# Kernel optimization log

Measured on AMD Instinct MI355X. Metric: run time of the kernel, lower is better.

Reference implementation:

```python
import jax, jax.numpy as jnp
import numpy as np

B, S, D, E, R = 8, 4096, 768, 8, 8

def setup_inputs() -> dict:
    key = jax.random.key(0)
    ks = jax.random.split(key, 9)
    sc = 0.02
    return {
        "x":  jax.random.normal(ks[0], (B, S, D), dtype=jnp.float32),
        "Wd": jax.random.normal(ks[1], (E, D, R), dtype=jnp.float32) * sc,
        "bd": jax.random.normal(ks[2], (E, R), dtype=jnp.float32) * sc,
        "Wm": jax.random.normal(ks[3], (E, R, R), dtype=jnp.float32) * sc,
        "bm": jax.random.normal(ks[4], (E, R), dtype=jnp.float32) * sc,
        "Wu": jax.random.normal(ks[5], (E, R, D), dtype=jnp.float32) * sc,
        "bu": jax.random.normal(ks[6], (E, D), dtype=jnp.float32) * sc,
        "Wg": jax.random.normal(ks[7], (D, E), dtype=jnp.float32) * sc,
        "bg": jax.random.normal(ks[8], (E,), dtype=jnp.float32) * sc,
    }

def reference(x, Wd, bd, Wm, bm, Wu, bu, Wg, bg):
    # Gating: softmax over experts. [B,S,E]
    gate = jax.nn.softmax(jnp.einsum('bsd,de->bse', x, Wg) + bg, axis=-1)
    # All experts batched as 3D GEMMs (dropout = identity, eval mode).
    h = jnp.einsum('bsd,edr->bser', x, Wd) + bd            # [B,S,E,R] down
    h = jnp.einsum('bser,erq->bseq', h, Wm) + bm           # [B,S,E,R] mid
    up = jnp.einsum('bser,erd->bsed', h, Wu) + bu          # [B,S,E,D] up
    # Weighted sum over experts.
    return jnp.einsum('bse,bsed->bsd', gate, up)
```

## Files before the change

kernel.cpp:

```cpp
#include <hip/hip_runtime.h>
#include <stdint.h>


typedef short bf16x8 __attribute__((ext_vector_type(8)));
typedef float f32x4 __attribute__((ext_vector_type(4)));

static __device__ __forceinline__ unsigned short f2bf(float f) {
  union { float f; uint32_t u; } v; v.f = f;
  return (unsigned short)((v.u + 0x7fffu + ((v.u >> 16) & 1u)) >> 16);
}

__global__ void prep_weights(const float* __restrict__ Wd, const float* __restrict__ Wg,
                             const float* __restrict__ Wu, const float* __restrict__ bu,
                             unsigned short* __restrict__ w1f, unsigned short* __restrict__ w2f) {
  int tid = blockIdx.x * 256 + threadIdx.x;
  const int N1 = 24 * 5 * 64 * 8;
  if (tid < N1) {
    int i    = tid & 7;
    int lane = (tid >> 3) & 63;
    int fk   = tid >> 9;
    int f = fk % 5, K0 = fk / 5;
    int k = K0 * 32 + (lane >> 4) * 8 + i;
    int j = f * 16 + (lane & 15);
    float val = 0.f;
    if (j < 64)      val = Wd[(size_t)(j >> 3) * 6144 + (size_t)k * 8 + (j & 7)];
    else if (j < 72) val = Wg[(size_t)k * 8 + (j - 64)];
    w1f[tid] = f2bf(val);
  } else {
    int t2 = tid - N1;
    if (t2 >= 48 * 3 * 64 * 8) return;
    int i    = t2 & 7;
    int lane = (t2 >> 3) & 63;
    int tk   = t2 >> 9;
    int K0 = tk % 3, T = tk / 3;
    int k = K0 * 32 + (lane >> 4) * 8 + i;
    int n = T * 16 + (lane & 15);
    float val = 0.f;
    if (k < 64)      val = Wu[(size_t)(k >> 3) * 6144 + (size_t)(k & 7) * 768 + n];
    else if (k < 72) val = bu[(size_t)(k - 64) * 768 + n];
    w2f[t2] = f2bf(val);
  }
}

__global__ __launch_bounds__(256, 8) void moba_fused(
    const float* __restrict__ x,
    const float* __restrict__ bd, const float* __restrict__ Wm,
    const float* __restrict__ bm, const float* __restrict__ bg,
    const unsigned short* __restrict__ w1f, const unsigned short* __restrict__ w2f,
    float* __restrict__ out) {
  __shared__ float Hs[4][16][81];
  __shared__ unsigned int g2s[16][52];

  const int tidx = threadIdx.x;
  const int lane = tidx & 63;
  const int wave = tidx >> 6;
  const int arow = lane & 15;
  const int kgrp = lane >> 4;
  const int tok0 = blockIdx.x * 16;

  {
    const float* xrow = x + (size_t)(tok0 + arow) * 768 + wave * 192 + kgrp * 8;
    f32x4 acc0 = {0,0,0,0}, acc1 = {0,0,0,0}, acc2 = {0,0,0,0}, acc3 = {0,0,0,0}, acc4 = {0,0,0,0};
    const bf16x8* w1v = (const bf16x8*)w1f + (size_t)(wave * 6) * 320 + lane;

    float4 xa[4][2];
    #pragma unroll
    for (int i = 0; i < 4; i++) {
      xa[i][0] = *(const float4*)(xrow + i * 32);
      xa[i][1] = *(const float4*)(xrow + i * 32 + 4);
    }
    #pragma unroll
    for (int i = 0; i < 6; i++) {
      float4 a0 = xa[i & 3][0];
      float4 a1 = xa[i & 3][1];
      if (i + 4 < 6) {
        xa[i & 3][0] = *(const float4*)(xrow + (i + 4) * 32);
        xa[i & 3][1] = *(const float4*)(xrow + (i + 4) * 32 + 4);
      }
      bf16x8 af;
      af[0] = (short)f2bf(a0.x); af[1] = (short)f2bf(a0.y);
      af[2] = (short)f2bf(a0.z); af[3] = (short)f2bf(a0.w);
      af[4] = (short)f2bf(a1.x); af[5] = (short)f2bf(a1.y);
      af[6] = (short)f2bf(a1.z); af[7] = (short)f2bf(a1.w);
      const bf16x8* bb = w1v + i * 320;
      acc0 = __builtin_amdgcn_mfma_f32_16x16x32_bf16(af, bb[0],   acc0, 0, 0, 0);
      acc1 = __builtin_amdgcn_mfma_f32_16x16x32_bf16(af, bb[64],  acc1, 0, 0, 0);
      acc2 = __builtin_amdgcn_mfma_f32_16x16x32_bf16(af, bb[128], acc2, 0, 0, 0);
      acc3 = __builtin_amdgcn_mfma_f32_16x16x32_bf16(af, bb[192], acc3, 0, 0, 0);
      acc4 = __builtin_amdgcn_mfma_f32_16x16x32_bf16(af, bb[256], acc4, 0, 0, 0);
    }
    int hr = kgrp * 4;
    #pragma unroll
    for (int r = 0; r < 4; r++) {
      Hs[wave][hr + r][arow]      = acc0[r];
      Hs[wave][hr + r][16 + arow] = acc1[r];
      Hs[wave][hr + r][32 + arow] = acc2[r];
      Hs[wave][hr + r][48 + arow] = acc3[r];
      Hs[wave][hr + r][64 + arow] = acc4[r];
    }
  }
  __syncthreads();

  if (tidx < 64) {
    int t = tidx >> 2;
    int c = tidx & 3;
    float lg[8];
    float m = -1e30f;
    #pragma unroll
    for (int e = 0; e < 8; e++) {
      lg[e] = Hs[0][t][64 + e] + Hs[1][t][64 + e] + Hs[2][t][64 + e] + Hs[3][t][64 + e] + bg[e];
      m = fmaxf(m, lg[e]);
    }
    float den = 0.f;
    #pragma unroll
    for (int e = 0; e < 8; e++) { lg[e] = __expf(lg[e] - m); den += lg[e]; }
    float inv = 1.f / den;
    #pragma unroll
    for (int ee = 0; ee < 2; ee++) {
      int e = c * 2 + ee;
      float gate = lg[e] * inv;
      float h[8];
      #pragma unroll
      for (int r = 0; r < 8; r++)
        h[r] = Hs[0][t][e * 8 + r] + Hs[1][t][e * 8 + r] + Hs[2][t][e * 8 + r] +
               Hs[3][t][e * 8 + r] + bd[e * 8 + r];
      #pragma unroll
      for (int q = 0; q < 8; q += 2) {
        float h2a = bm[e * 8 + q], h2b = bm[e * 8 + q + 1];
        #pragma unroll
        for (int r = 0; r < 8; r++) {
          h2a += h[r] * Wm[e * 64 + r * 8 + q];
          h2b += h[r] * Wm[e * 64 + r * 8 + q + 1];
        }
        g2s[t][e * 4 + (q >> 1)] =
            (unsigned)f2bf(gate * h2a) | ((unsigned)f2bf(gate * h2b) << 16);
      }
    }
    g2s[t][32 + c] = (unsigned)f2bf(lg[c * 2] * inv) | ((unsigned)f2bf(lg[c * 2 + 1] * inv) << 16);
    g2s[t][36 + c * 3 + 0] = 0;
    g2s[t][36 + c * 3 + 1] = 0;
    g2s[t][36 + c * 3 + 2] = 0;
  }
  __syncthreads();

  bf16x8 a2_0 = *(const bf16x8*)&g2s[arow][kgrp * 4];
  bf16x8 a2_1 = *(const bf16x8*)&g2s[arow][16 + kgrp * 4];
  bf16x8 a2_2 = *(const bf16x8*)&g2s[arow][32 + kgrp * 4];
  const bf16x8* w2v = (const bf16x8*)w2f + (size_t)(wave * 12) * 192 + lane;
  float* orow = out + (size_t)(tok0 + kgrp * 4) * 768 + arow + wave * 192;

  bf16x8 pb[4][3];
  #pragma unroll
  for (int d = 0; d < 4; d++) {
    pb[d][0] = w2v[d * 192];
    pb[d][1] = w2v[d * 192 + 64];
    pb[d][2] = w2v[d * 192 + 128];
  }
  #pragma unroll
  for (int j = 0; j < 12; j++) {
    bf16x8 b0 = pb[j & 3][0], b1 = pb[j & 3][1], b2 = pb[j & 3][2];
    if (j + 4 < 12) {
      pb[j & 3][0] = w2v[(j + 4) * 192];
      pb[j & 3][1] = w2v[(j + 4) * 192 + 64];
      pb[j & 3][2] = w2v[(j + 4) * 192 + 128];
    }
    f32x4 c2 = {0,0,0,0};
    c2 = __builtin_amdgcn_mfma_f32_16x16x32_bf16(a2_0, b0, c2, 0, 0, 0);
    c2 = __builtin_amdgcn_mfma_f32_16x16x32_bf16(a2_1, b1, c2, 0, 0, 0);
    c2 = __builtin_amdgcn_mfma_f32_16x16x32_bf16(a2_2, b2, c2, 0, 0, 0);
    #pragma unroll
    for (int r = 0; r < 4; r++)
      __builtin_nontemporal_store(c2[r], orow + (size_t)r * 768 + j * 16);
  }
}

extern "C" void kernel_launch(void* const* d_in, const int* in_sizes, int n_in,
                              void* d_out, int out_size, void* d_ws, size_t ws_size,
                              hipStream_t stream) {
  const float* x  = (const float*)d_in[0];
  const float* Wd = (const float*)d_in[1];
  const float* bd = (const float*)d_in[2];
  const float* Wm = (const float*)d_in[3];
  const float* bm = (const float*)d_in[4];
  const float* Wu = (const float*)d_in[5];
  const float* bu = (const float*)d_in[6];
  const float* Wg = (const float*)d_in[7];
  const float* bg = (const float*)d_in[8];
  unsigned short* w1f = (unsigned short*)d_ws;
  unsigned short* w2f = w1f + 61440;

  prep_weights<<<528, 256, 0, stream>>>(Wd, Wg, Wu, bu, w1f, w2f);
  moba_fused<<<2048, 256, 0, stream>>>(x, bd, Wm, bm, bg, w1f, w2f, (float*)d_out);
}
```

Baseline: 59.09 us.

## Split fused MoE adapter kernel into gate/down and up-projection kernels

Splits the single fused kernel into two launches: the first computes the down projection, gating softmax and mid layer, and writes gated bf16 activations to a workspace buffer in global memory. The second reads them back and runs the up-projection MFMAs. It also swaps the MFMA operand order so each lane writes a contiguous float4 of output with a regular store instead of strided nontemporal scalar stores. The intent is simpler per-kernel resource use and more coalesced output writes, at the cost of an extra launch and a global round trip for the intermediate.

```diff
diff --git a/kernel.cpp b/kernel.cpp
--- a/kernel.cpp
+++ b/kernel.cpp
@@ -42,14 +42,12 @@
   }
 }
 
-__global__ __launch_bounds__(256, 8) void moba_fused(
+__global__ __launch_bounds__(256) void k1_g2(
     const float* __restrict__ x,
     const float* __restrict__ bd, const float* __restrict__ Wm,
     const float* __restrict__ bm, const float* __restrict__ bg,
-    const unsigned short* __restrict__ w1f, const unsigned short* __restrict__ w2f,
-    float* __restrict__ out) {
+    const unsigned short* __restrict__ w1f, unsigned int* __restrict__ g2) {
   __shared__ float Hs[4][16][81];
-  __shared__ unsigned int g2s[16][52];
 
   const int tidx = threadIdx.x;
   const int lane = tidx & 63;
@@ -104,6 +102,7 @@
   if (tidx < 64) {
     int t = tidx >> 2;
     int c = tidx & 3;
+    unsigned int* g2u = g2 + (size_t)(tok0 + t) * 48;
     float lg[8];
     float m = -1e30f;
     #pragma unroll
@@ -132,22 +131,34 @@
           h2a += h[r] * Wm[e * 64 + r * 8 + q];
           h2b += h[r] * Wm[e * 64 + r * 8 + q + 1];
         }
-        g2s[t][e * 4 + (q >> 1)] =
+        g2u[e * 4 + (q >> 1)] =
             (unsigned)f2bf(gate * h2a) | ((unsigned)f2bf(gate * h2b) << 16);
       }
     }
-    g2s[t][32 + c] = (unsigned)f2bf(lg[c * 2] * inv) | ((unsigned)f2bf(lg[c * 2 + 1] * inv) << 16);
-    g2s[t][36 + c * 3 + 0] = 0;
-    g2s[t][36 + c * 3 + 1] = 0;
-    g2s[t][36 + c * 3 + 2] = 0;
-  }
-  __syncthreads();
-
-  bf16x8 a2_0 = *(const bf16x8*)&g2s[arow][kgrp * 4];
-  bf16x8 a2_1 = *(const bf16x8*)&g2s[arow][16 + kgrp * 4];
-  bf16x8 a2_2 = *(const bf16x8*)&g2s[arow][32 + kgrp * 4];
+    g2u[32 + c] = (unsigned)f2bf(lg[c * 2] * inv) | ((unsigned)f2bf(lg[c * 2 + 1] * inv) << 16);
+    g2u[36 + c * 3 + 0] = 0;
+    g2u[36 + c * 3 + 1] = 0;
+    g2u[36 + c * 3 + 2] = 0;
+  }
+}
+
+__global__ __launch_bounds__(256) void k2_out(
+    const unsigned short* __restrict__ g2bf, const unsigned short* __restrict__ w2f,
+    float* __restrict__ out) {
+  const int tidx = threadIdx.x;
+  const int lane = tidx & 63;
+  const int wave = tidx >> 6;
+  const int arow = lane & 15;
+  const int kgrp = lane >> 4;
+  const int tok0 = blockIdx.x * 16;
+
+  const unsigned short* grow = g2bf + (size_t)(tok0 + arow) * 96 + kgrp * 8;
+  bf16x8 a2_0 = *(const bf16x8*)(grow);
+  bf16x8 a2_1 = *(const bf16x8*)(grow + 32);
+  bf16x8 a2_2 = *(const bf16x8*)(grow + 64);
+
   const bf16x8* w2v = (const bf16x8*)w2f + (size_t)(wave * 12) * 192 + lane;
-  float* orow = out + (size_t)(tok0 + kgrp * 4) * 768 + arow + wave * 192;
+  float* orow = out + (size_t)(tok0 + arow) * 768 + wave * 192 + kgrp * 4;
 
   bf16x8 pb[4][3];
   #pragma unroll
@@ -165,12 +176,10 @@
       pb[j & 3][2] = w2v[(j + 4) * 192 + 128];
     }
     f32x4 c2 = {0,0,0,0};
-    c2 = __builtin_amdgcn_mfma_f32_16x16x32_bf16(a2_0, b0, c2, 0, 0, 0);
-    c2 = __builtin_amdgcn_mfma_f32_16x16x32_bf16(a2_1, b1, c2, 0, 0, 0);
-    c2 = __builtin_amdgcn_mfma_f32_16x16x32_bf16(a2_2, b2, c2, 0, 0, 0);
-    #pragma unroll
-    for (int r = 0; r < 4; r++)
-      __builtin_nontemporal_store(c2[r], orow + (size_t)r * 768 + j * 16);
+    c2 = __builtin_amdgcn_mfma_f32_16x16x32_bf16(b0, a2_0, c2, 0, 0, 0);
+    c2 = __builtin_amdgcn_mfma_f32_16x16x32_bf16(b1, a2_1, c2, 0, 0, 0);
+    c2 = __builtin_amdgcn_mfma_f32_16x16x32_bf16(b2, a2_2, c2, 0, 0, 0);
+    *(f32x4*)(orow + j * 16) = c2;
   }
 }
 
@@ -188,7 +197,9 @@
   const float* bg = (const float*)d_in[8];
   unsigned short* w1f = (unsigned short*)d_ws;
   unsigned short* w2f = w1f + 61440;
+  unsigned int*   g2  = (unsigned int*)((char*)d_ws + 270336);
 
   prep_weights<<<528, 256, 0, stream>>>(Wd, Wg, Wu, bu, w1f, w2f);
-  moba_fused<<<2048, 256, 0, stream>>>(x, bd, Wm, bm, bg, w1f, w2f, (float*)d_out);
-}
+  k1_g2<<<2048, 256, 0, stream>>>(x, bd, Wm, bm, bg, w1f, g2);
+  k2_out<<<2048, 256, 0, stream>>>((const unsigned short*)g2, w2f, (float*)d_out);
+}
```

New measurement: 64.82 us. 1.1x slower.

## Process two token tiles per block, prefetching next x tile during output GEMM

Applied to the files above, without the earlier changes.

Each block now handles 32 tokens as two 16-token stages. The second tile's x rows are loaded into registers before the first tile's up-projection runs, so the global-load latency overlaps MFMA work and output stores. The MFMA operands in the up-projection are swapped so each lane owns four contiguous output columns, which allows 16-byte vector stores instead of scalar nontemporal stores. The grid is halved and the occupancy hint in launch bounds is dropped, at the cost of more registers per thread and possibly fewer resident waves.

```diff
diff --git a/kernel.cpp b/kernel.cpp
--- a/kernel.cpp
+++ b/kernel.cpp
@@ -42,13 +42,13 @@
   }
 }
 
-__global__ __launch_bounds__(256, 8) void moba_fused(
+__global__ __launch_bounds__(256) void moba_pipe(
     const float* __restrict__ x,
     const float* __restrict__ bd, const float* __restrict__ Wm,
     const float* __restrict__ bm, const float* __restrict__ bg,
     const unsigned short* __restrict__ w1f, const unsigned short* __restrict__ w2f,
     float* __restrict__ out) {
-  __shared__ float Hs[4][16][81];
+  __shared__ float Hs[4][16][84];
   __shared__ unsigned int g2s[16][52];
 
   const int tidx = threadIdx.x;
@@ -56,27 +56,20 @@
   const int wave = tidx >> 6;
   const int arow = lane & 15;
   const int kgrp = lane >> 4;
-  const int tok0 = blockIdx.x * 16;
-
-  {
-    const float* xrow = x + (size_t)(tok0 + arow) * 768 + wave * 192 + kgrp * 8;
+  const int tok0 = blockIdx.x * 32;
+
+  const bf16x8* w1v = (const bf16x8*)w1f + (size_t)(wave * 6) * 320 + lane;
+  const bf16x8* w2v = (const bf16x8*)w2f + (size_t)(wave * 12) * 192 + lane;
+  const float*  xrow0 = x + (size_t)(tok0 + arow) * 768 + wave * 192 + kgrp * 8;
+
+  float4 xa[12];
+
+  auto computeA = [&]() {
     f32x4 acc0 = {0,0,0,0}, acc1 = {0,0,0,0}, acc2 = {0,0,0,0}, acc3 = {0,0,0,0}, acc4 = {0,0,0,0};
-    const bf16x8* w1v = (const bf16x8*)w1f + (size_t)(wave * 6) * 320 + lane;
-
-    float4 xa[4][2];
-    #pragma unroll
-    for (int i = 0; i < 4; i++) {
-      xa[i][0] = *(const float4*)(xrow + i * 32);
-      xa[i][1] = *(const float4*)(xrow + i * 32 + 4);
-    }
     #pragma unroll
     for (int i = 0; i < 6; i++) {
-      float4 a0 = xa[i & 3][0];
-      float4 a1 = xa[i & 3][1];
-      if (i + 4 < 6) {
-        xa[i & 3][0] = *(const float4*)(xrow + (i + 4) * 32);
-        xa[i & 3][1] = *(const float4*)(xrow + (i + 4) * 32 + 4);
-      }
+      float4 a0 = xa[2 * i];
+      float4 a1 = xa[2 * i + 1];
       bf16x8 af;
       af[0] = (short)f2bf(a0.x); af[1] = (short)f2bf(a0.y);
       af[2] = (short)f2bf(a0.z); af[3] = (short)f2bf(a0.w);
@@ -98,80 +91,107 @@
       Hs[wave][hr + r][48 + arow] = acc3[r];
       Hs[wave][hr + r][64 + arow] = acc4[r];
     }
+  };
+
+  auto middleB = [&](int s) {
+    if (tidx < 64) {
+      int t = tidx >> 2;
+      int c = tidx & 3;
+      float lg[8];
+      float m = -1e30f;
+      #pragma unroll
+      for (int e = 0; e < 8; e++) {
+        lg[e] = Hs[0][t][64 + e] + Hs[1][t][64 + e] + Hs[2][t][64 + e] + Hs[3][t][64 + e] + bg[e];
+        m = fmaxf(m, lg[e]);
+      }
+      float den = 0.f;
+      #pragma unroll
+      for (int e = 0; e < 8; e++) { lg[e] = __expf(lg[e] - m); den += lg[e]; }
+      float inv = 1.f / den;
+      unsigned int hv[8];
+      #pragma unroll
+      for (int ee = 0; ee < 2; ee++) {
+        int e = c * 2 + ee;
+        float gate = lg[e] * inv;
+        float h[8];
+        #pragma unroll
+        for (int r = 0; r < 8; r++)
+          h[r] = Hs[0][t][e * 8 + r] + Hs[1][t][e * 8 + r] + Hs[2][t][e * 8 + r] +
+                 Hs[3][t][e * 8 + r] + bd[e * 8 + r];
+        #pragma unroll
+        for (int q = 0; q < 8; q += 2) {
+          float h2a = bm[e * 8 + q], h2b = bm[e * 8 + q + 1];
+          #pragma unroll
+          for (int r = 0; r < 8; r++) {
+            h2a += h[r] * Wm[e * 64 + r * 8 + q];
+            h2b += h[r] * Wm[e * 64 + r * 8 + q + 1];
+          }
+          hv[ee * 4 + (q >> 1)] =
+              (unsigned)f2bf(gate * h2a) | ((unsigned)f2bf(gate * h2b) << 16);
+        }
+      }
+      *(uint4*)&g2s[t][8 * c]     = make_uint4(hv[0], hv[1], hv[2], hv[3]);
+      *(uint4*)&g2s[t][8 * c + 4] = make_uint4(hv[4], hv[5], hv[6], hv[7]);
+      g2s[t][32 + c] = (unsigned)f2bf(lg[c * 2] * inv) | ((unsigned)f2bf(lg[c * 2 + 1] * inv) << 16);
+      g2s[t][36 + c * 3 + 0] = 0;
+      g2s[t][36 + c * 3 + 1] = 0;
+      g2s[t][36 + c * 3 + 2] = 0;
+    }
+  };
+
+  auto phaseC = [&](int s) {
+    bf16x8 a2_0 = *(const bf16x8*)&g2s[arow][kgrp * 4];
+    bf16x8 a2_1 = *(const bf16x8*)&g2s[arow][16 + kgrp * 4];
+    bf16x8 a2_2 = *(const bf16x8*)&g2s[arow][32 + kgrp * 4];
+    float* orow = out + (size_t)(tok0 + s * 16 + arow) * 768 + wave * 192 + kgrp * 4;
+    bf16x8 pb[2][3];
+    #pragma unroll
+    for (int d = 0; d < 2; d++) {
+      pb[d][0] = w2v[d * 192];
+      pb[d][1] = w2v[d * 192 + 64];
+      pb[d][2] = w2v[d * 192 + 128];
+    }
+    #pragma unroll
+    for (int j = 0; j < 12; j++) {
+      bf16x8 b0 = pb[j & 1][0], b1 = pb[j & 1][1], b2 = pb[j & 1][2];
+      if (j + 2 < 12) {
+        pb[j & 1][0] = w2v[(j + 2) * 192];
+        pb[j & 1][1] = w2v[(j + 2) * 192 + 64];
+        pb[j & 1][2] = w2v[(j + 2) * 192 + 128];
+      }
+      f32x4 c2 = {0,0,0,0};
+      c2 = __builtin_amdgcn_mfma_f32_16x16x32_bf16(b0, a2_0, c2, 0, 0, 0);
+      c2 = __builtin_amdgcn_mfma_f32_16x16x32_bf16(b1, a2_1, c2, 0, 0, 0);
+      c2 = __builtin_amdgcn_mfma_f32_16x16x32_bf16(b2, a2_2, c2, 0, 0, 0);
+      *(f32x4*)(orow + j * 16) = c2;
+    }
+  };
+
+  #pragma unroll
+  for (int i = 0; i < 6; i++) {
+    xa[2 * i]     = *(const float4*)(xrow0 + i * 32);
+    xa[2 * i + 1] = *(const float4*)(xrow0 + i * 32 + 4);
   }
-  __syncthreads();
-
-  if (tidx < 64) {
-    int t = tidx >> 2;
-    int c = tidx & 3;
-    float lg[8];
-    float m = -1e30f;
-    #pragma unroll
-    for (int e = 0; e < 8; e++) {
-      lg[e] = Hs[0][t][64 + e] + Hs[1][t][64 + e] + Hs[2][t][64 + e] + Hs[3][t][64 + e] + bg[e];
-      m = fmaxf(m, lg[e]);
-    }
-    float den = 0.f;
-    #pragma unroll
-    for (int e = 0; e < 8; e++) { lg[e] = __expf(lg[e] - m); den += lg[e]; }
-    float inv = 1.f / den;
-    #pragma unroll
-    for (int ee = 0; ee < 2; ee++) {
-      int e = c * 2 + ee;
-      float gate = lg[e] * inv;
-      float h[8];
-      #pragma unroll
-      for (int r = 0; r < 8; r++)
-        h[r] = Hs[0][t][e * 8 + r] + Hs[1][t][e * 8 + r] + Hs[2][t][e * 8 + r] +
-               Hs[3][t][e * 8 + r] + bd[e * 8 + r];
-      #pragma unroll
-      for (int q = 0; q < 8; q += 2) {
-        float h2a = bm[e * 8 + q], h2b = bm[e * 8 + q + 1];
-        #pragma unroll
-        for (int r = 0; r < 8; r++) {
-          h2a += h[r] * Wm[e * 64 + r * 8 + q];
-          h2b += h[r] * Wm[e * 64 + r * 8 + q + 1];
-        }
-        g2s[t][e * 4 + (q >> 1)] =
-            (unsigned)f2bf(gate * h2a) | ((unsigned)f2bf(gate * h2b) << 16);
-      }
-    }
-    g2s[t][32 + c] = (unsigned)f2bf(lg[c * 2] * inv) | ((unsigned)f2bf(lg[c * 2 + 1] * inv) << 16);
-    g2s[t][36 + c * 3 + 0] = 0;
-    g2s[t][36 + c * 3 + 1] = 0;
-    g2s[t][36 + c * 3 + 2] = 0;
+  computeA();
+  __syncthreads();
+  middleB(0);
+  __syncthreads();
+
+  {
+    const float* xrow1 = xrow0 + (size_t)16 * 768;
+    #pragma unroll
+    for (int i = 0; i < 6; i++) {
+      xa[2 * i]     = *(const float4*)(xrow1 + i * 32);
+      xa[2 * i + 1] = *(const float4*)(xrow1 + i * 32 + 4);
+    }
   }
-  __syncthreads();
-
-  bf16x8 a2_0 = *(const bf16x8*)&g2s[arow][kgrp * 4];
-  bf16x8 a2_1 = *(const bf16x8*)&g2s[arow][16 + kgrp * 4];
-  bf16x8 a2_2 = *(const bf16x8*)&g2s[arow][32 + kgrp * 4];
-  const bf16x8* w2v = (const bf16x8*)w2f + (size_t)(wave * 12) * 192 + lane;
-  float* orow = out + (size_t)(tok0 + kgrp * 4) * 768 + arow + wave * 192;
-
-  bf16x8 pb[4][3];
-  #pragma unroll
-  for (int d = 0; d < 4; d++) {
-    pb[d][0] = w2v[d * 192];
-    pb[d][1] = w2v[d * 192 + 64];
-    pb[d][2] = w2v[d * 192 + 128];
-  }
-  #pragma unroll
-  for (int j = 0; j < 12; j++) {
-    bf16x8 b0 = pb[j & 3][0], b1 = pb[j & 3][1], b2 = pb[j & 3][2];
-    if (j + 4 < 12) {
-      pb[j & 3][0] = w2v[(j + 4) * 192];
-      pb[j & 3][1] = w2v[(j + 4) * 192 + 64];
-      pb[j & 3][2] = w2v[(j + 4) * 192 + 128];
-    }
-    f32x4 c2 = {0,0,0,0};
-    c2 = __builtin_amdgcn_mfma_f32_16x16x32_bf16(a2_0, b0, c2, 0, 0, 0);
-    c2 = __builtin_amdgcn_mfma_f32_16x16x32_bf16(a2_1, b1, c2, 0, 0, 0);
-    c2 = __builtin_amdgcn_mfma_f32_16x16x32_bf16(a2_2, b2, c2, 0, 0, 0);
-    #pragma unroll
-    for (int r = 0; r < 4; r++)
-      __builtin_nontemporal_store(c2[r], orow + (size_t)r * 768 + j * 16);
-  }
+  __builtin_amdgcn_sched_barrier(0);
+  phaseC(0);
+  computeA();
+  __syncthreads();
+  middleB(1);
+  __syncthreads();
+  phaseC(1);
 }
 
 extern "C" void kernel_launch(void* const* d_in, const int* in_sizes, int n_in,
@@ -190,5 +210,5 @@
   unsigned short* w2f = w1f + 61440;
 
   prep_weights<<<528, 256, 0, stream>>>(Wd, Wg, Wu, bu, w1f, w2f);
-  moba_fused<<<2048, 256, 0, stream>>>(x, bd, Wm, bm, bg, w1f, w2f, (float*)d_out);
-}
+  moba_pipe<<<1024, 256, 0, stream>>>(x, bd, Wm, bm, bg, w1f, w2f, (float*)d_out);
+}
```

Measured after the change: 96.82 us. 1.64x slower.

## Transpose second MFMA for vectorized float4 stores and loop two token tiles per block

Applied to the files above, without the earlier changes.

Operand order of the up-projection MFMA is swapped so each lane holds four consecutive output columns of one token, allowing 16-byte vector stores instead of four scalar nontemporal stores. The grid is halved and each block processes two 16-token tiles in a loop. The g2s writes become uint4 stores, the Hs padding changes, and the weight prefetch depth drops from 4 to 2. The launch-bounds occupancy hint is removed, and nontemporal stores are dropped, which may change cache behavior.

```diff
diff --git a/kernel.cpp b/kernel.cpp
--- a/kernel.cpp
+++ b/kernel.cpp
@@ -42,13 +42,13 @@
   }
 }
 
-__global__ __launch_bounds__(256, 8) void moba_fused(
+__global__ __launch_bounds__(256) void moba_conv(
     const float* __restrict__ x,
     const float* __restrict__ bd, const float* __restrict__ Wm,
     const float* __restrict__ bm, const float* __restrict__ bg,
     const unsigned short* __restrict__ w1f, const unsigned short* __restrict__ w2f,
     float* __restrict__ out) {
-  __shared__ float Hs[4][16][81];
+  __shared__ float Hs[4][16][84];
   __shared__ unsigned int g2s[16][52];
 
   const int tidx = threadIdx.x;
@@ -56,121 +56,129 @@
   const int wave = tidx >> 6;
   const int arow = lane & 15;
   const int kgrp = lane >> 4;
-  const int tok0 = blockIdx.x * 16;
-
-  {
-    const float* xrow = x + (size_t)(tok0 + arow) * 768 + wave * 192 + kgrp * 8;
-    f32x4 acc0 = {0,0,0,0}, acc1 = {0,0,0,0}, acc2 = {0,0,0,0}, acc3 = {0,0,0,0}, acc4 = {0,0,0,0};
-    const bf16x8* w1v = (const bf16x8*)w1f + (size_t)(wave * 6) * 320 + lane;
-
-    float4 xa[4][2];
-    #pragma unroll
-    for (int i = 0; i < 4; i++) {
-      xa[i][0] = *(const float4*)(xrow + i * 32);
-      xa[i][1] = *(const float4*)(xrow + i * 32 + 4);
+
+  for (int t = 0; t < 2; t++) {
+    const int tok0 = (blockIdx.x + t * 1024) * 16;
+
+    {
+      const float* xrow = x + (size_t)(tok0 + arow) * 768 + wave * 192 + kgrp * 8;
+      f32x4 acc0 = {0,0,0,0}, acc1 = {0,0,0,0}, acc2 = {0,0,0,0}, acc3 = {0,0,0,0}, acc4 = {0,0,0,0};
+      const bf16x8* w1v = (const bf16x8*)w1f + (size_t)(wave * 6) * 320 + lane;
+
+      float4 xa[4][2];
+      #pragma unroll
+      for (int i = 0; i < 4; i++) {
+        xa[i][0] = *(const float4*)(xrow + i * 32);
+        xa[i][1] = *(const float4*)(xrow + i * 32 + 4);
+      }
+      #pragma unroll
+      for (int i = 0; i < 6; i++) {
+        float4 a0 = xa[i & 3][0];
+        float4 a1 = xa[i & 3][1];
+        if (i + 4 < 6) {
+          xa[i & 3][0] = *(const float4*)(xrow + (i + 4) * 32);
+          xa[i & 3][1] = *(const float4*)(xrow + (i + 4) * 32 + 4);
+        }
+        bf16x8 af;
+        af[0] = (short)f2bf(a0.x); af[1] = (short)f2bf(a0.y);
+        af[2] = (short)f2bf(a0.z); af[3] = (short)f2bf(a0.w);
+        af[4] = (short)f2bf(a1.x); af[5] = (short)f2bf(a1.y);
+        af[6] = (short)f2bf(a1.z); af[7] = (short)f2bf(a1.w);
+        const bf16x8* bb = w1v + i * 320;
+        acc0 = __builtin_amdgcn_mfma_f32_16x16x32_bf16(af, bb[0],   acc0, 0, 0, 0);
+        acc1 = __builtin_amdgcn_mfma_f32_16x16x32_bf16(af, bb[64],  acc1, 0, 0, 0);
+        acc2 = __builtin_amdgcn_mfma_f32_16x16x32_bf16(af, bb[128], acc2, 0, 0, 0);
+        acc3 = __builtin_amdgcn_mfma_f32_16x16x32_bf16(af, bb[192], acc3, 0, 0, 0);
+        acc4 = __builtin_amdgcn_mfma_f32_16x16x32_bf16(af, bb[256], acc4, 0, 0, 0);
+      }
+      int hr = kgrp * 4;
+      #pragma unroll
+      for (int r = 0; r < 4; r++) {
+        Hs[wave][hr + r][arow]      = acc0[r];
+        Hs[wave][hr + r][16 + arow] = acc1[r];
+        Hs[wave][hr + r][32 + arow] = acc2[r];
+        Hs[wave][hr + r][48 + arow] = acc3[r];
+        Hs[wave][hr + r][64 + arow] = acc4[r];
+      }
     }
-    #pragma unroll
-    for (int i = 0; i < 6; i++) {
-      float4 a0 = xa[i & 3][0];
-      float4 a1 = xa[i & 3][1];
-      if (i + 4 < 6) {
-        xa[i & 3][0] = *(const float4*)(xrow + (i + 4) * 32);
-        xa[i & 3][1] = *(const float4*)(xrow + (i + 4) * 32 + 4);
-      }
-      bf16x8 af;
-      af[0] = (short)f2bf(a0.x); af[1] = (short)f2bf(a0.y);
-      af[2] = (short)f2bf(a0.z); af[3] = (short)f2bf(a0.w);
-      af[4] = (short)f2bf(a1.x); af[5] = (short)f2bf(a1.y);
-      af[6] = (short)f2bf(a1.z); af[7] = (short)f2bf(a1.w);
-      const bf16x8* bb = w1v + i * 320;
-      acc0 = __builtin_amdgcn_mfma_f32_16x16x32_bf16(af, bb[0],   acc0, 0, 0, 0);
-      acc1 = __builtin_amdgcn_mfma_f32_16x16x32_bf16(af, bb[64],  acc1, 0, 0, 0);
-      acc2 = __builtin_amdgcn_mfma_f32_16x16x32_bf16(af, bb[128], acc2, 0, 0, 0);
-      acc3 = __builtin_amdgcn_mfma_f32_16x16x32_bf16(af, bb[192], acc3, 0, 0, 0);
-      acc4 = __builtin_amdgcn_mfma_f32_16x16x32_bf16(af, bb[256], acc4, 0, 0, 0);
+    __syncthreads();
+
+    if (tidx < 64) {
+      int tt = tidx >> 2;
+      int c  = tidx & 3;
+      float lg[8];
+      float m = -1e30f;
+      #pragma unroll
+      for (int e = 0; e < 8; e++) {
+        lg[e] = Hs[0][tt][64 + e] + Hs[1][tt][64 + e] + Hs[2][tt][64 + e] + Hs[3][tt][64 + e] + bg[e];
+        m = fmaxf(m, lg[e]);
+      }
+      float den = 0.f;
+      #pragma unroll
+      for (int e = 0; e < 8; e++) { lg[e] = __expf(lg[e] - m); den += lg[e]; }
+      float inv = 1.f / den;
+      unsigned int hv[8];
+      #pragma unroll
+      for (int ee = 0; ee < 2; ee++) {
+        int e = c * 2 + ee;
+        float gate = lg[e] * inv;
+        float h[8];
+        #pragma unroll
+        for (int r = 0; r < 8; r++)
+          h[r] = Hs[0][tt][e * 8 + r] + Hs[1][tt][e * 8 + r] + Hs[2][tt][e * 8 + r] +
+                 Hs[3][tt][e * 8 + r] + bd[e * 8 + r];
+        #pragma unroll
+        for (int q = 0; q < 8; q += 2) {
+          float h2a = bm[e * 8 + q], h2b = bm[e * 8 + q + 1];
+          #pragma unroll
+          for (int r = 0; r < 8; r++) {
+            h2a += h[r] * Wm[e * 64 + r * 8 + q];
+            h2b += h[r] * Wm[e * 64 + r * 8 + q + 1];
+          }
+          hv[ee * 4 + (q >> 1)] =
+              (unsigned)f2bf(gate * h2a) | ((unsigned)f2bf(gate * h2b) << 16);
+        }
+      }
+      *(uint4*)&g2s[tt][8 * c]     = make_uint4(hv[0], hv[1], hv[2], hv[3]);
+      *(uint4*)&g2s[tt][8 * c + 4] = make_uint4(hv[4], hv[5], hv[6], hv[7]);
+      g2s[tt][32 + c] = (unsigned)f2bf(lg[c * 2] * inv) | ((unsigned)f2bf(lg[c * 2 + 1] * inv) << 16);
+      g2s[tt][36 + c * 3 + 0] = 0;
+      g2s[tt][36 + c * 3 + 1] = 0;
+      g2s[tt][36 + c * 3 + 2] = 0;
     }
-    int hr = kgrp * 4;
-    #pragma unroll
-    for (int r = 0; r < 4; r++) {
-      Hs[wave][hr + r][arow]      = acc0[r];
-      Hs[wave][hr + r][16 + arow] = acc1[r];
-      Hs[wave][hr + r][32 + arow] = acc2[r];
-      Hs[wave][hr + r][48 + arow] = acc3[r];
-      Hs[wave][hr + r][64 + arow] = acc4[r];
+    __syncthreads();
+
+    {
+      bf16x8 a2_0 = *(const bf16x8*)&g2s[arow][kgrp * 4];
+      bf16x8 a2_1 = *(const bf16x8*)&g2s[arow][16 + kgrp * 4];
+      bf16x8 a2_2 = *(const bf16x8*)&g2s[arow][32 + kgrp * 4];
+
+      const bf16x8* w2v = (const bf16x8*)w2f + (size_t)(wave * 12) * 192 + lane;
+      float* orow = out + (size_t)(tok0 + arow) * 768 + wave * 192 + kgrp * 4;
+
+      bf16x8 pb[2][3];
+      #pragma unroll
+      for (int d = 0; d < 2; d++) {
+        pb[d][0] = w2v[d * 192];
+        pb[d][1] = w2v[d * 192 + 64];
+        pb[d][2] = w2v[d * 192 + 128];
+      }
+      #pragma unroll
+      for (int j = 0; j < 12; j++) {
+        bf16x8 b0 = pb[j & 1][0], b1 = pb[j & 1][1], b2 = pb[j & 1][2];
+        if (j + 2 < 12) {
+          pb[j & 1][0] = w2v[(j + 2) * 192];
+          pb[j & 1][1] = w2v[(j + 2) * 192 + 64];
+          pb[j & 1][2] = w2v[(j + 2) * 192 + 128];
+        }
+        f32x4 c2 = {0,0,0,0};
+        c2 = __builtin_amdgcn_mfma_f32_16x16x32_bf16(b0, a2_0, c2, 0, 0, 0);
+        c2 = __builtin_amdgcn_mfma_f32_16x16x32_bf16(b1, a2_1, c2, 0, 0, 0);
+        c2 = __builtin_amdgcn_mfma_f32_16x16x32_bf16(b2, a2_2, c2, 0, 0, 0);
+        *(f32x4*)(orow + j * 16) = c2;
+      }
     }
-  }
-  __syncthreads();
-
-  if (tidx < 64) {
-    int t = tidx >> 2;
-    int c = tidx & 3;
-    float lg[8];
-    float m = -1e30f;
-    #pragma unroll
-    for (int e = 0; e < 8; e++) {
-      lg[e] = Hs[0][t][64 + e] + Hs[1][t][64 + e] + Hs[2][t][64 + e] + Hs[3][t][64 + e] + bg[e];
-      m = fmaxf(m, lg[e]);
-    }
-    float den = 0.f;
-    #pragma unroll
-    for (int e = 0; e < 8; e++) { lg[e] = __expf(lg[e] - m); den += lg[e]; }
-    float inv = 1.f / den;
-    #pragma unroll
-    for (int ee = 0; ee < 2; ee++) {
-      int e = c * 2 + ee;
-      float gate = lg[e] * inv;
-      float h[8];
-      #pragma unroll
-      for (int r = 0; r < 8; r++)
-        h[r] = Hs[0][t][e * 8 + r] + Hs[1][t][e * 8 + r] + Hs[2][t][e * 8 + r] +
-               Hs[3][t][e * 8 + r] + bd[e * 8 + r];
-      #pragma unroll
-      for (int q = 0; q < 8; q += 2) {
-        float h2a = bm[e * 8 + q], h2b = bm[e * 8 + q + 1];
-        #pragma unroll
-        for (int r = 0; r < 8; r++) {
-          h2a += h[r] * Wm[e * 64 + r * 8 + q];
-          h2b += h[r] * Wm[e * 64 + r * 8 + q + 1];
-        }
-        g2s[t][e * 4 + (q >> 1)] =
-            (unsigned)f2bf(gate * h2a) | ((unsigned)f2bf(gate * h2b) << 16);
-      }
-    }
-    g2s[t][32 + c] = (unsigned)f2bf(lg[c * 2] * inv) | ((unsigned)f2bf(lg[c * 2 + 1] * inv) << 16);
-    g2s[t][36 + c * 3 + 0] = 0;
-    g2s[t][36 + c * 3 + 1] = 0;
-    g2s[t][36 + c * 3 + 2] = 0;
-  }
-  __syncthreads();
-
-  bf16x8 a2_0 = *(const bf16x8*)&g2s[arow][kgrp * 4];
-  bf16x8 a2_1 = *(const bf16x8*)&g2s[arow][16 + kgrp * 4];
-  bf16x8 a2_2 = *(const bf16x8*)&g2s[arow][32 + kgrp * 4];
-  const bf16x8* w2v = (const bf16x8*)w2f + (size_t)(wave * 12) * 192 + lane;
-  float* orow = out + (size_t)(tok0 + kgrp * 4) * 768 + arow + wave * 192;
-
-  bf16x8 pb[4][3];
-  #pragma unroll
-  for (int d = 0; d < 4; d++) {
-    pb[d][0] = w2v[d * 192];
-    pb[d][1] = w2v[d * 192 + 64];
-    pb[d][2] = w2v[d * 192 + 128];
-  }
-  #pragma unroll
-  for (int j = 0; j < 12; j++) {
-    bf16x8 b0 = pb[j & 3][0], b1 = pb[j & 3][1], b2 = pb[j & 3][2];
-    if (j + 4 < 12) {
-      pb[j & 3][0] = w2v[(j + 4) * 192];
-      pb[j & 3][1] = w2v[(j + 4) * 192 + 64];
-      pb[j & 3][2] = w2v[(j + 4) * 192 + 128];
-    }
-    f32x4 c2 = {0,0,0,0};
-    c2 = __builtin_amdgcn_mfma_f32_16x16x32_bf16(a2_0, b0, c2, 0, 0, 0);
-    c2 = __builtin_amdgcn_mfma_f32_16x16x32_bf16(a2_1, b1, c2, 0, 0, 0);
-    c2 = __builtin_amdgcn_mfma_f32_16x16x32_bf16(a2_2, b2, c2, 0, 0, 0);
-    #pragma unroll
-    for (int r = 0; r < 4; r++)
-      __builtin_nontemporal_store(c2[r], orow + (size_t)r * 768 + j * 16);
+    if (t == 0) __syncthreads();
   }
 }
 
@@ -190,5 +198,5 @@
   unsigned short* w2f = w1f + 61440;
 
   prep_weights<<<528, 256, 0, stream>>>(Wd, Wg, Wu, bu, w1f, w2f);
-  moba_fused<<<2048, 256, 0, stream>>>(x, bd, Wm, bm, bg, w1f, w2f, (float*)d_out);
-}
+  moba_conv<<<1024, 256, 0, stream>>>(x, bd, Wm, bm, bg, w1f, w2f, (float*)d_out);
+}
```

After: 79.86 us. 35.2% more time.
